# Kernel tuning notes

Hardware: AMD Instinct MI355X
Metric: run time of the kernel (lower is better)

## Reference

```python
import jax, jax.numpy as jnp
import numpy as np

B, S, D = 2, 2048, 2048
NH, NKV, DH = 16, 4, 128
NG = NH // NKV  # query heads per kv head


def rope_apply(x, cos, sin):
    # x: [B, H, S, DH]; cos/sin: [S, DH//2]
    x1, x2 = jnp.split(x, 2, axis=-1)
    c = cos[None, None, :, :]
    s = sin[None, None, :, :]
    return jnp.concatenate([x1 * c - x2 * s, x1 * s + x2 * c], axis=-1)


def setup_inputs() -> dict:
    key = jax.random.key(0)
    ks = jax.random.split(key, 6)
    x = jax.random.normal(ks[0], (B, S, D), dtype=jnp.float32)
    # real RoPE frequencies
    inv_freq = 1.0 / (10000.0 ** (jnp.arange(0, DH // 2, dtype=jnp.float32) * 2.0 / DH))
    angles = jnp.arange(S, dtype=jnp.float32)[:, None] * inv_freq[None, :]  # [S, DH//2]
    cos, sin = jnp.cos(angles), jnp.sin(angles)
    mask = jnp.tril(jnp.ones((S, S), dtype=bool))[None, None]  # causal [1,1,S,S]
    sc = 0.02
    Wq = jax.random.normal(ks[1], (D, NH * DH), dtype=jnp.float32) * sc
    Wk = jax.random.normal(ks[2], (D, NKV * DH), dtype=jnp.float32) * sc
    Wv = jax.random.normal(ks[3], (D, NKV * DH), dtype=jnp.float32) * sc
    Wo = jax.random.normal(ks[4], (NH * DH, D), dtype=jnp.float32) * sc
    return {"x": x, "cos": cos, "sin": sin, "mask": mask,
            "Wq": Wq, "Wk": Wk, "Wv": Wv, "Wo": Wo}


def reference(x, cos, sin, mask, Wq, Wk, Wv, Wo):
    b, s, _ = x.shape
    q = (x @ Wq).reshape(b, s, NH, DH).transpose(0, 2, 1, 3)    # [B,NH,S,DH]
    k = (x @ Wk).reshape(b, s, NKV, DH).transpose(0, 2, 1, 3)   # [B,NKV,S,DH]
    v = (x @ Wv).reshape(b, s, NKV, DH).transpose(0, 2, 1, 3)
    q = rope_apply(q, cos, sin)
    k = rope_apply(k, cos, sin)
    new_kv_cache = (k, v)
    k_exp = jnp.repeat(k, NG, axis=1)  # [B,NH,S,DH]
    v_exp = jnp.repeat(v, NG, axis=1)
    scale = jnp.float32(np.sqrt(DH))
    scores = jnp.einsum('bhqd,bhkd->bhqk', q, k_exp) / scale
    scores = jnp.where(mask, scores, jnp.float32(-1e9))
    weights = jax.nn.softmax(scores, axis=-1)
    context = jnp.einsum('bhqk,bhkd->bhqd', weights, v_exp)
    context = context.transpose(0, 2, 1, 3).reshape(b, s, NH * DH)
    output = context @ Wo
    return output, new_kv_cache[0], new_kv_cache[1]
```

## Files before the change

### kernel.cpp

```cpp
#include <hip/hip_runtime.h>
#include <stdint.h>

#define Bb 2
#define Ss 2048
#define Dd 2048
#define NHh 16
#define NKVv 4
#define DHh 128
#define Mm_ (Bb*Ss)
#define NQq (NHh*DHh)

using bf16x8 = __attribute__((ext_vector_type(8))) __bf16;
using f32x4  = __attribute__((ext_vector_type(4))) float;

__device__ __forceinline__ unsigned short f2bf(float f) {
  unsigned u = __float_as_uint(f);
  u += 0x7fffu + ((u >> 16) & 1u);
  return (unsigned short)(u >> 16);
}
__device__ __forceinline__ float bf2f(unsigned short s) {
  return __uint_as_float(((unsigned)s) << 16);
}

__global__ void k_convert(const float* __restrict__ in, unsigned short* __restrict__ out, int n4) {
  const int i = blockIdx.x * blockDim.x + threadIdx.x;
  if (i >= n4) return;
  const float4 v = ((const float4*)in)[i];
  ushort4 o;
  o.x = f2bf(v.x); o.y = f2bf(v.y); o.z = f2bf(v.z); o.w = f2bf(v.w);
  ((ushort4*)out)[i] = o;
}

__global__ __launch_bounds__(256) void k_transpose_all(
    const float* __restrict__ Wq, const float* __restrict__ Wk,
    const float* __restrict__ Wv, const float* __restrict__ Wo,
    unsigned short* __restrict__ wqkvT, unsigned short* __restrict__ woT) {
  __shared__ float tile[32][33];
  int bid = blockIdx.x;
  const float* in;
  unsigned short* out;
  int Nn;
  if (bid < 4096)      { in = Wq; out = wqkvT;                        Nn = 2048; }
  else if (bid < 5120) { in = Wk; out = wqkvT + (size_t)2048 * 2048;  Nn = 512;  bid -= 4096; }
  else if (bid < 6144) { in = Wv; out = wqkvT + (size_t)2560 * 2048;  Nn = 512;  bid -= 5120; }
  else                 { in = Wo; out = woT;                          Nn = 2048; bid -= 6144; }
  const int nbx = Nn >> 5;
  const int n0 = (bid % nbx) * 32, k0 = (bid / nbx) * 32;
  const int tx = threadIdx.x & 31, ty = threadIdx.x >> 5;
  #pragma unroll
  for (int i = 0; i < 4; ++i)
    tile[ty + i * 8][tx] = in[(size_t)(k0 + ty + i * 8) * Nn + n0 + tx];
  __syncthreads();
  #pragma unroll
  for (int i = 0; i < 4; ++i)
    out[(size_t)(n0 + ty + i * 8) * 2048 + k0 + tx] = f2bf(tile[tx][ty + i * 8]);
}

template<int BNW, int MODE>
__global__ __launch_bounds__(512) void k_gemm256(const unsigned short* __restrict__ A,
                                                 const unsigned short* __restrict__ BT,
                                                 int Kdim,
                                                 unsigned short* __restrict__ Qo,
                                                 float* __restrict__ kfo,
                                                 float* __restrict__ outV,
                                                 unsigned short* __restrict__ vTb,
                                                 float* __restrict__ Cf) {
  __shared__ unsigned short ldsA[2][16384];
  __shared__ unsigned short ldsB[2][4096 * BNW];
  const int tid = threadIdx.x;
  const int lane = tid & 63;
  const int lg = lane >> 4, ll = lane & 15;
  const int wid = tid >> 6;
  const int wm = wid >> 2, wn = wid & 3;
  const int m0 = blockIdx.y << 8;
  const int n0 = blockIdx.x * (64 * BNW);

  f32x4 acc[8][BNW] = {};
  bf16x8 bfr[BNW];

  auto stage_A = [&](int buf, int kt, int s) {
    const int c = (s << 9) + tid;
    const int row = c >> 3, c16 = c & 7;
    const int csrc = (c16 ^ (row & 7)) << 3;
    const unsigned short* src = A + (size_t)(m0 + row) * Kdim + kt * 64 + csrc;
    __builtin_amdgcn_global_load_lds(
        (const __attribute__((address_space(1))) void*)src,
        (__attribute__((address_space(3))) void*)(&ldsA[buf][0] + c * 8), 16, 0, 0);
  };
  auto stage_B = [&](int buf, int kt, int s) {
    const int c = (s << 9) + tid;
    const int row = c >> 3, c16 = c & 7;
    const int csrc = (c16 ^ (row & 7)) << 3;
    const unsigned short* src = BT + (size_t)(n0 + row) * Kdim + kt * 64 + csrc;
    __builtin_amdgcn_global_load_lds(
        (const __attribute__((address_space(1))) void*)src,
        (__attribute__((address_space(3))) void*)(&ldsB[buf][0] + c * 8), 16, 0, 0);
  };

  #pragma unroll
  for (int s = 0; s < 4; ++s) stage_A(0, 0, s);
  #pragma unroll
  for (int s = 0; s < BNW; ++s) stage_B(0, 0, s);
  __syncthreads();

  const int nkt = Kdim >> 6;
  int cur = 0;
  for (int kt = 0; kt < nkt; ++kt) {
    const int nxt = cur ^ 1;
    const bool hn = (kt + 1 < nkt);
    const char* Atl = (const char*)&ldsA[cur][0];
    const char* Btl = (const char*)&ldsB[cur][0];

    auto rdB = [&](int ks) {
      #pragma unroll
      for (int i = 0; i < BNW; ++i) {
        const int r = wn * (16 * BNW) + i * 16 + ll;
        bfr[i] = *(const bf16x8*)(const void*)(
            Btl + r * 128 + ((ks * 64 + lg * 16) ^ ((r & 7) << 4)));
      }
    };
    auto quad = [&](int mh, int ks) {
      bf16x8 af[4];
      #pragma unroll
      for (int i = 0; i < 4; ++i) {
        const int r = wm * 128 + (mh * 4 + i) * 16 + ll;
        af[i] = *(const bf16x8*)(const void*)(
            Atl + r * 128 + ((ks * 64 + lg * 16) ^ ((r & 7) << 4)));
      }
      __builtin_amdgcn_s_setprio(1);
      #pragma unroll
      for (int i = 0; i < 4; ++i)
        #pragma unroll
        for (int n = 0; n < BNW; ++n)
          acc[mh * 4 + i][n] =
              __builtin_amdgcn_mfma_f32_16x16x32_bf16(af[i], bfr[n], acc[mh * 4 + i][n], 0, 0, 0);
      __builtin_amdgcn_s_setprio(0);
    };

    rdB(0);
    if (hn) { stage_A(nxt, kt + 1, 0); stage_A(nxt, kt + 1, 1);
              stage_A(nxt, kt + 1, 2); stage_A(nxt, kt + 1, 3); }
    __builtin_amdgcn_s_barrier();
    quad(0, 0);
    __builtin_amdgcn_s_barrier();
    if (hn) {
      #pragma unroll
      for (int s = 0; s < BNW; ++s) stage_B(nxt, kt + 1, s);
    }
    __builtin_amdgcn_s_barrier();
    quad(1, 0);
    __builtin_amdgcn_s_barrier();
    rdB(1);
    __builtin_amdgcn_s_barrier();
    quad(0, 1);
    __builtin_amdgcn_s_barrier();
    quad(1, 1);
    if (hn) {
      asm volatile("s_waitcnt vmcnt(0)" ::: "memory");
    }
    __builtin_amdgcn_s_barrier();
    cur ^= 1;
  }

  #pragma unroll
  for (int mi = 0; mi < 8; ++mi)
    #pragma unroll
    for (int ni = 0; ni < BNW; ++ni) {
      const int row4 = m0 + wm * 128 + mi * 16 + lg * 4;
      const int col = n0 + wn * (16 * BNW) + ni * 16 + ll;
      if (MODE == 1) {
        #pragma unroll
        for (int jj = 0; jj < 4; ++jj)
          Cf[(size_t)(row4 + jj) * 2048 + col] = acc[mi][ni][jj];
      } else {
        if (col < 2048) {
          #pragma unroll
          for (int jj = 0; jj < 4; ++jj)
            Qo[(size_t)(row4 + jj) * 2048 + col] = f2bf(acc[mi][ni][jj]);
        } else if (col < 2560) {
          #pragma unroll
          for (int jj = 0; jj < 4; ++jj)
            kfo[(size_t)(row4 + jj) * 512 + (col - 2048)] = acc[mi][ni][jj];
        } else {
          const int kv = (col - 2560) >> 7, dh = (col - 2560) & 127;
          const int b = row4 >> 11, s0 = row4 & 2047;
          #pragma unroll
          for (int jj = 0; jj < 4; ++jj)
            outV[((size_t)(b * NKVv + kv) * Ss + s0 + jj) * DHh + dh] = acc[mi][ni][jj];
          ushort4 pk;
          pk.x = f2bf(acc[mi][ni][0]); pk.y = f2bf(acc[mi][ni][1]);
          pk.z = f2bf(acc[mi][ni][2]); pk.w = f2bf(acc[mi][ni][3]);
          *(ushort4*)&vTb[((size_t)(b * NKVv + kv) * DHh + dh) * Ss + s0] = pk;
        }
      }
    }
}

__global__ void k_rope_k(const float* __restrict__ kf, const float* __restrict__ cosT,
                         const float* __restrict__ sinT, float* __restrict__ outK,
                         unsigned short* __restrict__ kbb) {
  const int idx = blockIdx.x * blockDim.x + threadIdx.x;
  if (idx >= Mm_ * NKVv * 64) return;
  const int dh2 = idx & 63;
  const int kv = (idx >> 6) & 3;
  const int m = idx >> 8;
  const int s = m & (Ss - 1);
  const int b = m >> 11;
  const size_t src = (size_t)m * 512 + kv * DHh + dh2;
  const float x1 = kf[src], x2 = kf[src + 64];
  const float c = cosT[s * 64 + dh2], sn = sinT[s * 64 + dh2];
  const float o1 = x1 * c - x2 * sn, o2 = x1 * sn + x2 * c;
  const size_t dst = ((size_t)(b * NKVv + kv) * Ss + s) * DHh + dh2;
  outK[dst] = o1; outK[dst + 64] = o2;
  kbb[dst] = f2bf(o1); kbb[dst + 64] = f2bf(o2);
}

__global__ __launch_bounds__(128) void k_attn(const unsigned short* __restrict__ qb,
                                              const unsigned short* __restrict__ kb,
                                              const unsigned short* __restrict__ vT,
                                              const float* __restrict__ cosT,
                                              const float* __restrict__ sinT,
                                              unsigned short* __restrict__ ctxb) {
  const int linear = blockIdx.y * 64 + blockIdx.x;
  const int r = linear >> 8;
  const int u = linear & 255;
  const int q3 = u & 7;
  const int bh = u >> 3;
  int qq;
  if (r & 1) qq = 63 - (((r >> 1) << 3) + q3);
  else       qq = ((r >> 1) << 3) + q3;

  const int b = bh >> 4, h = bh & 15;
  const int kvh = h >> 2;
  const int tid = threadIdx.x, wid = tid >> 6, lane = tid & 63;
  const int lg = lane >> 4, ll = lane & 15;
  __shared__ unsigned short kts[32 * 128];
  __shared__ unsigned short vts[128 * 32];
  __shared__ unsigned short p_s[1024];
  const char* ktc = (const char*)kts;
  const char* vtc = (const char*)vts;
  char* pwc = (char*)p_s + wid * 1024;
  const int swzk = (ll & 7) << 4;
  const int swz4 = (ll & 3) << 4;
  const unsigned short* kbase = kb + (size_t)(b * NKVv + kvh) * Ss * DHh;
  const unsigned short* vbase = vT + (size_t)(b * NKVv + kvh) * DHh * Ss;
  const int qrow_f = qq * 32 + wid * 16 + ll;
  const unsigned short* qrow = qb + (size_t)(b * Ss + qrow_f) * NQq + h * DHh;

  uint4 rq[4];
  #pragma unroll
  for (int ks = 0; ks < 4; ++ks)
    rq[ks] = *(const uint4*)(const void*)(qrow + ks * 32 + lg * 8);
  bf16x8 qfr[4];
  {
    const unsigned short* rqs = (const unsigned short*)rq;
    unsigned short qtmp[4][8];
    const float scq = 0.12751746595544662f;
    #pragma unroll
    for (int ksh = 0; ksh < 2; ++ksh) {
      #pragma unroll
      for (int e = 0; e < 8; ++e) {
        const int dh2 = ksh * 32 + lg * 8 + e;
        const float c = cosT[qrow_f * 64 + dh2], sn = sinT[qrow_f * 64 + dh2];
        const float x1 = bf2f(rqs[ksh * 8 + e]);
        const float x2 = bf2f(rqs[(ksh + 2) * 8 + e]);
        qtmp[ksh][e]     = f2bf((x1 * c - x2 * sn) * scq);
        qtmp[ksh + 2][e] = f2bf((x1 * sn + x2 * c) * scq);
      }
    }
    #pragma unroll
    for (int ks = 0; ks < 4; ++ks) qfr[ks] = *(const bf16x8*)(const void*)qtmp[ks];
  }

  union { unsigned int u4[4]; bf16x8 v; } onesu;
  onesu.u4[0] = onesu.u4[1] = onesu.u4[2] = onesu.u4[3] = 0x3F803F80u;
  const bf16x8 onesf = onesu.v;

  f32x4 ctx[9] = {};
  const int qr0 = qq * 32 + wid * 16 + lg * 4;
  const int nkt = qq + 1;

  auto stage_k = [&](int ktile) {
    #pragma unroll
    for (int i = 0; i < 4; ++i) {
      const int c = i * 128 + tid;
      const int krow = c >> 4, kc = c & 15;
      const int kcs = (kc ^ (krow & 7)) << 3;
      const unsigned short* ksrc = kbase + (size_t)(ktile * 32 + krow) * DHh + kcs;
      __builtin_amdgcn_global_load_lds(
          (const __attribute__((address_space(1))) void*)ksrc,
          (__attribute__((address_space(3))) void*)(kts + (i * 128 + wid * 64) * 8), 16, 0, 0);
    }
  };
  auto stage_v = [&](int ktile) {
    #pragma unroll
    for (int i = 0; i < 4; ++i) {
      const int c = i * 128 + tid;
      const int vrow = c >> 2, vc = c & 3;
      const int vcs = (vc ^ (vrow & 3)) << 3;
      const unsigned short* vsrc = vbase + (size_t)vrow * Ss + ktile * 32 + vcs;
      __builtin_amdgcn_global_load_lds(
          (const __attribute__((address_space(1))) void*)vsrc,
          (__attribute__((address_space(3))) void*)(vts + (i * 128 + wid * 64) * 8), 16, 0, 0);
    }
  };

  stage_k(0);
  __syncthreads();
  for (int kt = 0; kt < nkt; ++kt) {
    stage_v(kt);
    f32x4 sc[2] = {};
    __builtin_amdgcn_s_setprio(1);
    #pragma unroll
    for (int ks = 0; ks < 4; ++ks) {
      #pragma unroll
      for (int cb = 0; cb < 2; ++cb) {
        const bf16x8 kfr = *(const bf16x8*)(const void*)(
            ktc + ((cb * 16 + ll) << 8) + (((ks << 6) + (lg << 4)) ^ swzk));
        sc[cb] = __builtin_amdgcn_mfma_f32_16x16x32_bf16(qfr[ks], kfr, sc[cb], 0, 0, 0);
      }
    }
    __builtin_amdgcn_s_setprio(0);
    const bool domask = (kt == qq);
    float pv[2][4];
    #pragma unroll
    for (int cb = 0; cb < 2; ++cb)
      #pragma unroll
      for (int j = 0; j < 4; ++j) {
        float s = sc[cb][j];
        if (domask && (kt * 32 + cb * 16 + ll > qr0 + j)) s = -1e30f;
        pv[cb][j] = exp2f(s - 8.656170245333781f);
      }
    #pragma unroll
    for (int cb = 0; cb < 2; ++cb)
      #pragma unroll
      for (int j = 0; j < 4; ++j) {
        const int prow = lg * 4 + j;
        *(unsigned short*)(pwc + (prow << 6) + (((cb << 5) + (ll << 1)) ^ ((prow & 3) << 4))) =
            (unsigned short)((__float_as_uint(pv[cb][j]) + 0x8000u) >> 16);
      }
    __syncthreads();
    if (kt + 1 < nkt) stage_k(kt + 1);
    __builtin_amdgcn_s_setprio(1);
    {
      const bf16x8 pa = *(const bf16x8*)(const void*)(
          pwc + (ll << 6) + ((lg << 4) ^ swz4));
      #pragma unroll
      for (int ob = 0; ob < 8; ++ob) {
        const bf16x8 vfr = *(const bf16x8*)(const void*)(
            vtc + ((ob * 16 + ll) << 6) + ((lg << 4) ^ swz4));
        ctx[ob] = __builtin_amdgcn_mfma_f32_16x16x32_bf16(pa, vfr, ctx[ob], 0, 0, 0);
      }
      ctx[8] = __builtin_amdgcn_mfma_f32_16x16x32_bf16(pa, onesf, ctx[8], 0, 0, 0);
    }
    __builtin_amdgcn_s_setprio(0);
    __syncthreads();
  }
  #pragma unroll
  for (int j = 0; j < 4; ++j) {
    const float inv = 1.f / ctx[8][j];
    unsigned short* crow = ctxb + (size_t)(b * Ss + qr0 + j) * NQq + h * DHh;
    #pragma unroll
    for (int ob = 0; ob < 8; ++ob)
      crow[ob * 16 + ll] = f2bf(ctx[ob][j] * inv);
  }
}

extern "C" void kernel_launch(void* const* d_in, const int* in_sizes, int n_in,
                              void* d_out, int out_size, void* d_ws, size_t ws_size,
                              hipStream_t stream) {
  const float* x    = (const float*)d_in[0];
  const float* cosT = (const float*)d_in[1];
  const float* sinT = (const float*)d_in[2];
  const float* Wq   = (const float*)d_in[4];
  const float* Wk   = (const float*)d_in[5];
  const float* Wv   = (const float*)d_in[6];
  const float* Wo   = (const float*)d_in[7];
  float* out  = (float*)d_out;
  float* outK = out + (size_t)Mm_ * Dd;
  float* outV = outK + (size_t)Bb * NKVv * Ss * DHh;

  char* ws = (char*)d_ws;
  size_t off = 0;
  auto alloc = [&](size_t bytes) -> void* {
    void* p = ws + off;
    off += (bytes + 255) & ~(size_t)255;
    return p;
  };
  unsigned short* xb    = (unsigned short*)alloc((size_t)Mm_ * Dd * 2);
  unsigned short* wqkvT = (unsigned short*)alloc((size_t)3072 * Dd * 2);
  unsigned short* woT   = (unsigned short*)alloc((size_t)Dd * NQq * 2);
  unsigned short* qfb   = (unsigned short*)alloc((size_t)Mm_ * NQq * 2);
  float*          kf    = (float*)alloc((size_t)Mm_ * 512 * 4);
  unsigned short* kbb   = (unsigned short*)alloc((size_t)Bb * NKVv * Ss * DHh * 2);
  unsigned short* vTb   = (unsigned short*)alloc((size_t)Bb * NKVv * Ss * DHh * 2);
  unsigned short* ctxb  = (unsigned short*)alloc((size_t)Mm_ * NQq * 2);
  if (off > ws_size) return;

  k_convert<<<(Mm_ * Dd / 4 + 255) / 256, 256, 0, stream>>>(x, xb, Mm_ * Dd / 4);
  k_transpose_all<<<10240, 256, 0, stream>>>(Wq, Wk, Wv, Wo, wqkvT, woT);
  k_gemm256<3, 0><<<dim3(16, 16), 512, 0, stream>>>(
      xb, wqkvT, Dd, qfb, kf, outV, vTb, (float*)nullptr);
  k_rope_k<<<(Mm_ * NKVv * 64 + 255) / 256, 256, 0, stream>>>(kf, cosT, sinT, outK, kbb);
  k_attn<<<dim3(64, 32), 128, 0, stream>>>(qfb, kbb, vTb, cosT, sinT, ctxb);
  k_gemm256<2, 1><<<dim3(16, 16), 512, 0, stream>>>(
      ctxb, woT, NQq, (unsigned short*)nullptr, (float*)nullptr,
      (float*)nullptr, (unsigned short*)nullptr, out);
}
```

Before: 199.3 us.

## Use 64-row query tiles with 4 waves and double-buffered K/V staging

The attention kernel now has 256-thread blocks, each covering 64 query rows instead of 32, so every staged K/V tile is shared by four waves. K and V tiles are double-buffered, and the next tile is prefetched while the current one is computed, which leaves one barrier per iteration instead of two. Waves whose rows lie entirely before a key tile skip its compute, and the block schedule is remapped to balance the causal work. In exchange the kernel uses more shared memory per block, runs fewer blocks, and has idle waves on the diagonal tiles.

```diff
diff --git a/kernel.cpp b/kernel.cpp
--- a/kernel.cpp
+++ b/kernel.cpp
@@ -215,36 +215,37 @@
   kbb[dst] = f2bf(o1); kbb[dst + 64] = f2bf(o2);
 }
 
-__global__ __launch_bounds__(128) void k_attn(const unsigned short* __restrict__ qb,
+__global__ __launch_bounds__(256) void k_attn(const unsigned short* __restrict__ qb,
                                               const unsigned short* __restrict__ kb,
                                               const unsigned short* __restrict__ vT,
                                               const float* __restrict__ cosT,
                                               const float* __restrict__ sinT,
                                               unsigned short* __restrict__ ctxb) {
-  const int linear = blockIdx.y * 64 + blockIdx.x;
+  const int linear = blockIdx.y * 32 + blockIdx.x;
   const int r = linear >> 8;
   const int u = linear & 255;
-  const int q3 = u & 7;
+  const int q2 = u & 7;
   const int bh = u >> 3;
-  int qq;
-  if (r & 1) qq = 63 - (((r >> 1) << 3) + q3);
-  else       qq = ((r >> 1) << 3) + q3;
+  int qt;
+  if      (r == 0) qt = q2;
+  else if (r == 1) qt = 15 - q2;
+  else if (r == 2) qt = 16 + q2;
+  else             qt = 31 - q2;
 
   const int b = bh >> 4, h = bh & 15;
   const int kvh = h >> 2;
   const int tid = threadIdx.x, wid = tid >> 6, lane = tid & 63;
   const int lg = lane >> 4, ll = lane & 15;
-  __shared__ unsigned short kts[32 * 128];
-  __shared__ unsigned short vts[128 * 32];
-  __shared__ unsigned short p_s[1024];
-  const char* ktc = (const char*)kts;
-  const char* vtc = (const char*)vts;
+  __shared__ unsigned short kts[2][4096];
+  __shared__ unsigned short vts[2][4096];
+  __shared__ unsigned short p_s[2048];
   char* pwc = (char*)p_s + wid * 1024;
   const int swzk = (ll & 7) << 4;
   const int swz4 = (ll & 3) << 4;
   const unsigned short* kbase = kb + (size_t)(b * NKVv + kvh) * Ss * DHh;
   const unsigned short* vbase = vT + (size_t)(b * NKVv + kvh) * DHh * Ss;
-  const int qrow_f = qq * 32 + wid * 16 + ll;
+  const int qbw = qt * 64 + wid * 16;
+  const int qrow_f = qbw + ll;
   const unsigned short* qrow = qb + (size_t)(b * Ss + qrow_f) * NQq + h * DHh;
 
   uint4 rq[4];
@@ -277,84 +278,84 @@
   const bf16x8 onesf = onesu.v;
 
   f32x4 ctx[9] = {};
-  const int qr0 = qq * 32 + wid * 16 + lg * 4;
-  const int nkt = qq + 1;
-
-  auto stage_k = [&](int ktile) {
-    #pragma unroll
-    for (int i = 0; i < 4; ++i) {
-      const int c = i * 128 + tid;
+  const int qr0 = qbw + lg * 4;
+  const int nkt = 2 * qt + 2;
+
+  auto stage_k = [&](int ktile, int bi) {
+    #pragma unroll
+    for (int i = 0; i < 2; ++i) {
+      const int c = i * 256 + tid;
       const int krow = c >> 4, kc = c & 15;
       const int kcs = (kc ^ (krow & 7)) << 3;
       const unsigned short* ksrc = kbase + (size_t)(ktile * 32 + krow) * DHh + kcs;
       __builtin_amdgcn_global_load_lds(
           (const __attribute__((address_space(1))) void*)ksrc,
-          (__attribute__((address_space(3))) void*)(kts + (i * 128 + wid * 64) * 8), 16, 0, 0);
+          (__attribute__((address_space(3))) void*)(&kts[bi][0] + (i * 256 + wid * 64) * 8), 16, 0, 0);
     }
   };
-  auto stage_v = [&](int ktile) {
-    #pragma unroll
-    for (int i = 0; i < 4; ++i) {
-      const int c = i * 128 + tid;
+  auto stage_v = [&](int ktile, int bi) {
+    #pragma unroll
+    for (int i = 0; i < 2; ++i) {
+      const int c = i * 256 + tid;
       const int vrow = c >> 2, vc = c & 3;
       const int vcs = (vc ^ (vrow & 3)) << 3;
       const unsigned short* vsrc = vbase + (size_t)vrow * Ss + ktile * 32 + vcs;
       __builtin_amdgcn_global_load_lds(
           (const __attribute__((address_space(1))) void*)vsrc,
-          (__attribute__((address_space(3))) void*)(vts + (i * 128 + wid * 64) * 8), 16, 0, 0);
+          (__attribute__((address_space(3))) void*)(&vts[bi][0] + (i * 256 + wid * 64) * 8), 16, 0, 0);
     }
   };
 
-  stage_k(0);
+  stage_k(0, 0);
+  stage_v(0, 0);
   __syncthreads();
+  int cur = 0;
   for (int kt = 0; kt < nkt; ++kt) {
-    stage_v(kt);
-    f32x4 sc[2] = {};
-    __builtin_amdgcn_s_setprio(1);
-    #pragma unroll
-    for (int ks = 0; ks < 4; ++ks) {
-      #pragma unroll
-      for (int cb = 0; cb < 2; ++cb) {
-        const bf16x8 kfr = *(const bf16x8*)(const void*)(
-            ktc + ((cb * 16 + ll) << 8) + (((ks << 6) + (lg << 4)) ^ swzk));
-        sc[cb] = __builtin_amdgcn_mfma_f32_16x16x32_bf16(qfr[ks], kfr, sc[cb], 0, 0, 0);
-      }
-    }
-    __builtin_amdgcn_s_setprio(0);
-    const bool domask = (kt == qq);
-    float pv[2][4];
-    #pragma unroll
-    for (int cb = 0; cb < 2; ++cb)
-      #pragma unroll
-      for (int j = 0; j < 4; ++j) {
-        float s = sc[cb][j];
-        if (domask && (kt * 32 + cb * 16 + ll > qr0 + j)) s = -1e30f;
-        pv[cb][j] = exp2f(s - 8.656170245333781f);
-      }
-    #pragma unroll
-    for (int cb = 0; cb < 2; ++cb)
-      #pragma unroll
-      for (int j = 0; j < 4; ++j) {
-        const int prow = lg * 4 + j;
-        *(unsigned short*)(pwc + (prow << 6) + (((cb << 5) + (ll << 1)) ^ ((prow & 3) << 4))) =
-            (unsigned short)((__float_as_uint(pv[cb][j]) + 0x8000u) >> 16);
-      }
+    if (kt + 1 < nkt) { stage_k(kt + 1, cur ^ 1); stage_v(kt + 1, cur ^ 1); }
+    const bool active = (kt * 32 <= qbw + 15);
+    if (active) {
+      const char* ktc = (const char*)&kts[cur][0];
+      const char* vtc = (const char*)&vts[cur][0];
+      f32x4 sc[2] = {};
+      __builtin_amdgcn_s_setprio(1);
+      #pragma unroll
+      for (int ks = 0; ks < 4; ++ks) {
+        #pragma unroll
+        for (int cb = 0; cb < 2; ++cb) {
+          const bf16x8 kfr = *(const bf16x8*)(const void*)(
+              ktc + ((cb * 16 + ll) << 8) + (((ks << 6) + (lg << 4)) ^ swzk));
+          sc[cb] = __builtin_amdgcn_mfma_f32_16x16x32_bf16(qfr[ks], kfr, sc[cb], 0, 0, 0);
+        }
+      }
+      __builtin_amdgcn_s_setprio(0);
+      const bool domask = (kt * 32 + 31 > qbw);
+      #pragma unroll
+      for (int cb = 0; cb < 2; ++cb)
+        #pragma unroll
+        for (int j = 0; j < 4; ++j) {
+          float s = sc[cb][j];
+          if (domask && (kt * 32 + cb * 16 + ll > qr0 + j)) s = -1e30f;
+          const float p = exp2f(s - 8.656170245333781f);
+          const int prow = lg * 4 + j;
+          *(unsigned short*)(pwc + (prow << 6) + (((cb << 5) + (ll << 1)) ^ ((prow & 3) << 4))) =
+              (unsigned short)((__float_as_uint(p) + 0x8000u) >> 16);
+        }
+      __builtin_amdgcn_s_setprio(1);
+      {
+        const bf16x8 pa = *(const bf16x8*)(const void*)(
+            pwc + (ll << 6) + ((lg << 4) ^ swz4));
+        #pragma unroll
+        for (int ob = 0; ob < 8; ++ob) {
+          const bf16x8 vfr = *(const bf16x8*)(const void*)(
+              vtc + ((ob * 16 + ll) << 6) + ((lg << 4) ^ swz4));
+          ctx[ob] = __builtin_amdgcn_mfma_f32_16x16x32_bf16(pa, vfr, ctx[ob], 0, 0, 0);
+        }
+        ctx[8] = __builtin_amdgcn_mfma_f32_16x16x32_bf16(pa, onesf, ctx[8], 0, 0, 0);
+      }
+      __builtin_amdgcn_s_setprio(0);
+    }
     __syncthreads();
-    if (kt + 1 < nkt) stage_k(kt + 1);
-    __builtin_amdgcn_s_setprio(1);
-    {
-      const bf16x8 pa = *(const bf16x8*)(const void*)(
-          pwc + (ll << 6) + ((lg << 4) ^ swz4));
-      #pragma unroll
-      for (int ob = 0; ob < 8; ++ob) {
-        const bf16x8 vfr = *(const bf16x8*)(const void*)(
-            vtc + ((ob * 16 + ll) << 6) + ((lg << 4) ^ swz4));
-        ctx[ob] = __builtin_amdgcn_mfma_f32_16x16x32_bf16(pa, vfr, ctx[ob], 0, 0, 0);
-      }
-      ctx[8] = __builtin_amdgcn_mfma_f32_16x16x32_bf16(pa, onesf, ctx[8], 0, 0, 0);
-    }
-    __builtin_amdgcn_s_setprio(0);
-    __syncthreads();
+    cur ^= 1;
   }
   #pragma unroll
   for (int j = 0; j < 4; ++j) {
@@ -402,7 +403,7 @@
   k_gemm256<3, 0><<<dim3(16, 16), 512, 0, stream>>>(
       xb, wqkvT, Dd, qfb, kf, outV, vTb, (float*)nullptr);
   k_rope_k<<<(Mm_ * NKVv * 64 + 255) / 256, 256, 0, stream>>>(kf, cosT, sinT, outK, kbb);
-  k_attn<<<dim3(64, 32), 128, 0, stream>>>(qfb, kbb, vTb, cosT, sinT, ctxb);
+  k_attn<<<dim3(32, 32), 256, 0, stream>>>(qfb, kbb, vTb, cosT, sinT, ctxb);
   k_gemm256<2, 1><<<dim3(16, 16), 512, 0, stream>>>(
       ctxb, woT, NQq, (unsigned short*)nullptr, (float*)nullptr,
       (float*)nullptr, (unsigned short*)nullptr, out);
```

Measured after the change: 207.4 us. 1.04x slower.
